# Kernel tuning notes

Measured on AMD Instinct MI355X. Metric: run time of the kernel, lower is better.

## Reference

```python
import jax, jax.numpy as jnp
import numpy as np

N_EMBED = 1024
CUTOFFS = [20000, 60000, 180000]
N_VOCAB = 267735
BOUNDS = [0] + CUTOFFS + [N_VOCAB]            # cluster boundaries
N_EMBEDS = [1024, 256, 64, 16]                # n_embed / 4**i
N_TOK = 1024
N_CLUSTERS = len(CUTOFFS)                      # 3 tail clusters


def setup_inputs() -> dict:
    key = jax.random.key(0)
    ks = jax.random.split(key, 12)

    def w(k, shape):
        fan_in = shape[0]
        return (jax.random.normal(k, shape, jnp.float32) / np.sqrt(fan_in)).astype(jnp.float32)

    inp = {}
    inp["hidden"] = jax.random.normal(ks[0], (N_TOK, N_EMBED), jnp.float32)
    inp["target"] = jax.random.randint(ks[1], (N_TOK,), 0, N_VOCAB)
    # head: layers[0] = Linear(n_embed, cutoffs[0]); clusters = Linear(n_embed, n_clusters)
    inp["W_head"] = w(ks[2], (N_EMBED, BOUNDS[1]))
    inp["b_head"] = jnp.zeros((BOUNDS[1],), jnp.float32)
    inp["W_cluster"] = w(ks[3], (N_EMBED, N_CLUSTERS))
    inp["b_cluster"] = jnp.zeros((N_CLUSTERS,), jnp.float32)
    # tails: projections[i-1] = Linear(n_embed, n_embeds[i], bias=False); layers[i] = Linear(n_embeds[i], end-start)
    for i in range(1, N_CLUSTERS + 1):
        size = BOUNDS[i + 1] - BOUNDS[i]
        inp[f"W_proj{i}"] = w(ks[3 + 2 * i], (N_EMBED, N_EMBEDS[i]))
        inp[f"W_tail{i}"] = w(ks[4 + 2 * i], (N_EMBEDS[i], size))
        inp[f"b_tail{i}"] = jnp.zeros((size,), jnp.float32)
    return inp


def _adaptive_nll(hidden, target, W_head, b_head, W_cluster, b_cluster, tails):
    # head logits = [vocab cluster 0 | cluster logits], then log_softmax (matches torch.cat + log_softmax)
    head_logit = jnp.concatenate(
        [hidden @ W_head + b_head, hidden @ W_cluster + b_cluster], axis=1)  # [N, cut0 + n_clusters]
    head_lp = jax.nn.log_softmax(head_logit, axis=1)

    # cluster 0: logprob = head_lp[n, target]
    t0 = jnp.clip(target, 0, BOUNDS[1] - 1)
    lp0 = jnp.take_along_axis(head_lp, t0[:, None], axis=1)[:, 0]
    nll = jnp.where(target < BOUNDS[1], -lp0, jnp.zeros((), head_lp.dtype))

    # tail clusters i=1..3: logprob = head_lp[:, -i] + tail_log_softmax[n, target-start]
    for i, (Wp, Wt, bt) in enumerate(tails, start=1):
        start, end = BOUNDS[i], BOUNDS[i + 1]
        tail_lp = jax.nn.log_softmax((hidden @ Wp) @ Wt + bt, axis=1)  # [N, end-start]
        rel = jnp.clip(target - start, 0, end - start - 1)
        lp_i = head_lp[:, -i] + jnp.take_along_axis(tail_lp, rel[:, None], axis=1)[:, 0]
        in_bucket = (target >= start) & (target < end)
        nll = jnp.where(in_bucket, -lp_i, nll)
    return nll  # [N], per-token negative log-likelihood (keep_order=True semantics)


def reference(hidden, target, W_head, b_head, W_cluster, b_cluster,
              W_proj1, W_tail1, b_tail1,
              W_proj2, W_tail2, b_tail2,
              W_proj3, W_tail3, b_tail3):
    tails = [(W_proj1, W_tail1, b_tail1),
             (W_proj2, W_tail2, b_tail2),
             (W_proj3, W_tail3, b_tail3)]
    return _adaptive_nll(hidden, target, W_head, b_head, W_cluster, b_cluster, tails)
```

## Files before the change

kernel.cpp:

```cpp
#include <hip/hip_runtime.h>
#include <cstdint>
#include <cstddef>


typedef unsigned short u16;
typedef __attribute__((ext_vector_type(8))) __bf16 bf16x8;
typedef __attribute__((ext_vector_type(8))) u16 u16x8;
typedef __attribute__((ext_vector_type(4))) float f32x4;

#define AS1 __attribute__((address_space(1)))
#define AS3 __attribute__((address_space(3)))

__device__ __forceinline__ u16 f2bf(float f){
  union { float f; unsigned u; } v; v.f = f;
  unsigned r = v.u + 0x7fffu + ((v.u >> 16) & 1u);
  return (u16)(r >> 16);
}
__device__ __forceinline__ void glds16(const void* g, void* l){
  __builtin_amdgcn_global_load_lds((AS1 unsigned*)(uintptr_t)g,
                                   (AS3 unsigned*)(unsigned)(uintptr_t)l, 16, 0, 0);
}

__global__ void k_init(int* __restrict__ cnt, int* __restrict__ trel){
  int i = blockIdx.x * 256 + threadIdx.x;
  trel[i] = -1;
  if (i < 4) cnt[i] = 0;
}

struct TJob { const float* W; u16* BT; int K, N, Kpad, nrows, nx, base, blk; };
struct TJobs { TJob j[8]; int nj; };

template<int TPB>
__device__ __forceinline__ void transpose_tile(const TJobs& jobs, int id,
                                               float (*t)[65], int tid){
  int ji = 0;
  #pragma unroll
  for (int i = 1; i < 8; ++i)
    if (i < jobs.nj && id >= jobs.j[i].base) ji = i;
  TJob jb = jobs.j[ji];
  int local = id - jb.base;
  int bx = local % jb.nx;
  int by = local / jb.nx;

  const int n0 = bx * 64;
  const int k0 = by * 64;
  const bool al = (jb.N & 3) == 0;
  for (int i = tid; i < 64*16; i += TPB){
    int r = i >> 4, c4 = (i & 15) * 4;
    int k = k0 + r, n = n0 + c4;
    f32x4 v; v.x=0.f; v.y=0.f; v.z=0.f; v.w=0.f;
    if (k < jb.K){
      if (al && n + 3 < jb.N) v = *(const f32x4*)(jb.W + (size_t)k * jb.N + n);
      else { for (int q = 0; q < 4; ++q) if (n + q < jb.N) v[q] = jb.W[(size_t)k * jb.N + n + q]; }
    }
    t[r][c4] = v.x; t[r][c4+1] = v.y; t[r][c4+2] = v.z; t[r][c4+3] = v.w;
  }
  __syncthreads();
  for (int i = tid; i < 64*8; i += TPB){
    int rn = i >> 3, c8 = (i & 7) * 8;
    int n = n0 + rn;
    if (k0 + c8 < jb.Kpad && n < jb.nrows){
      u16x8 o;
      #pragma unroll
      for (int q = 0; q < 8; ++q) o[q] = f2bf(t[c8 + q][rn]);
      size_t off;
      if (jb.blk)
        off = (((size_t)(n >> 7) * (jb.Kpad >> 6) + (k0 >> 6)) * 128 + (n & 127)) * 64 + c8;
      else
        off = (size_t)n * jb.Kpad + k0 + c8;
      *(u16x8*)(jb.BT + off) = o;
    }
  }
}

__global__ void k_stage1(TJobs jobs, int nbT, int ncvt,
                         const float* __restrict__ h, u16* __restrict__ a0,
                         const int* __restrict__ tgt, int* __restrict__ cnt,
                         int* __restrict__ idx1, int* __restrict__ idx2,
                         int* __restrict__ idx3, int* __restrict__ pos,
                         int* __restrict__ tr0, int* __restrict__ tr1,
                         int* __restrict__ tr2, int* __restrict__ tr3){
  __shared__ float t[64][65];
  const int bid = blockIdx.x, tid = threadIdx.x;
  if (bid < nbT){
    transpose_tile<256>(jobs, bid, t, tid);
  } else if (bid < nbT + ncvt){
    int i = ((bid - nbT) * 256 + tid) * 8;
    f32x4 v0 = *(const f32x4*)(h + i);
    f32x4 v1 = *(const f32x4*)(h + i + 4);
    u16x8 o;
    o[0]=f2bf(v0.x); o[1]=f2bf(v0.y); o[2]=f2bf(v0.z); o[3]=f2bf(v0.w);
    o[4]=f2bf(v1.x); o[5]=f2bf(v1.y); o[6]=f2bf(v1.z); o[7]=f2bf(v1.w);
    *(u16x8*)(a0 + i) = o;
  } else {
    int n = (bid - nbT - ncvt) * 256 + tid;
    int tv = tgt[n];
    int p = 0;
    tr0[n] = (tv < 20000) ? tv : -1;
    if (tv >= 20000){
      int b = (tv < 60000) ? 0 : (tv < 180000 ? 1 : 2);
      p = atomicAdd(&cnt[b], 1);
      if (b == 0){ idx1[p] = n; tr1[p] = tv - 20000; }
      else if (b == 1){ idx2[p] = n; tr2[p] = tv - 60000; }
      else { idx3[p] = n; tr3[p] = tv - 180000; }
    }
    pos[n] = p;
  }
}

__device__ __forceinline__
void proj_body(const u16* __restrict__ A, const u16* __restrict__ BT,
               const float* __restrict__ bc,
               u16* __restrict__ A1, u16* __restrict__ A2,
               u16* __restrict__ A3, float* __restrict__ cl,
               int pm, int pn, u16* As, u16* Bs)
{
  constexpr int BK = 64, K = 1024;
  const int tid  = threadIdx.x;
  const int lane = tid & 63, wid = tid >> 6;
  const int wm = wid & 3, wn = wid >> 2;
  const int l15 = lane & 15, l4 = lane >> 4;
  const int m0 = pm * 256;
  const int n0 = pn * 128;

  f32x4 acc[4][4];
  #pragma unroll
  for (int m = 0; m < 4; ++m)
    #pragma unroll
    for (int n = 0; n < 4; ++n){ acc[m][n].x=0.f; acc[m][n].y=0.f; acc[m][n].z=0.f; acc[m][n].w=0.f; }

  for (int kt = 0; kt < K / BK; ++kt){
    #pragma unroll
    for (int i = 0; i < 4; ++i){
      int c = wid * 4 + i;
      int row = c * 8 + lane / 8, kb = lane % 8;
      glds16((const char*)(A + (size_t)(m0 + row) * K + kt * BK) + kb * 16,
             (char*)As + c * 1024);
    }
    #pragma unroll
    for (int i = 0; i < 2; ++i){
      int c = wid * 2 + i;
      int row = c * 8 + lane / 8, kb = lane % 8;
      glds16((const char*)(BT + (size_t)(n0 + row) * K + kt * BK) + kb * 16,
             (char*)Bs + c * 1024);
    }
    __syncthreads();
    #pragma unroll
    for (int ks = 0; ks < 2; ++ks){
      bf16x8 af[4], bfr[4];
      #pragma unroll
      for (int m = 0; m < 4; ++m)
        af[m] = *(const bf16x8*)((const char*)As + (wm*64 + m*16 + l15) * (BK*2) + ks*64 + l4*16);
      #pragma unroll
      for (int n = 0; n < 4; ++n)
        bfr[n] = *(const bf16x8*)((const char*)Bs + (wn*64 + n*16 + l15) * (BK*2) + ks*64 + l4*16);
      #pragma unroll
      for (int m = 0; m < 4; ++m)
        #pragma unroll
        for (int n = 0; n < 4; ++n)
          acc[m][n] = __builtin_amdgcn_mfma_f32_16x16x32_bf16(af[m], bfr[n], acc[m][n], 0, 0, 0);
    }
    __syncthreads();
  }
  #pragma unroll
  for (int m = 0; m < 4; ++m)
    #pragma unroll
    for (int n = 0; n < 4; ++n)
      #pragma unroll
      for (int q = 0; q < 4; ++q){
        int c = n0 + wn*64 + n*16 + l15;
        int r = m0 + wm*64 + m*16 + l4*4 + q;
        float v = acc[m][n][q];
        if (c < 256)      A1[(size_t)r*256 + c] = f2bf(v);
        else if (c < 320) A2[(size_t)r*64 + (c-256)] = f2bf(v);
        else if (c < 336){ u16* p = A3 + (size_t)r*32 + (c-320);
                           p[0] = f2bf(v); p[16] = 0; }
        else if (c < 339) cl[(size_t)r*3 + (c-336)] = v + bc[c-336];
      }
}

__device__ __forceinline__
void gemm256_body(const u16* __restrict__ A, const u16* __restrict__ BT,
                  const float* __restrict__ bias, int K, int N,
                  float* __restrict__ P, int ntiles, int cb, int rb,
                  const int* __restrict__ tgt_rel, float* __restrict__ tl,
                  u16* As, u16* Bs, float* reds, int* trel_s)
{
  constexpr int BK = 64;
  const int tid  = threadIdx.x;
  const int lane = tid & 63, wid = tid >> 6;
  const int wm = wid & 3, wn = wid >> 2;
  const int l15 = lane & 15, l4 = lane >> 4;
  const int m0 = rb * 256;
  const int n0 = cb * 128;
  const int srow = lane >> 3, skb = lane & 7;

  if (tid < 256) trel_s[tid] = tgt_rel[m0 + tid];

  f32x4 acc[4][4];
  #pragma unroll
  for (int m = 0; m < 4; ++m)
    #pragma unroll
    for (int n = 0; n < 4; ++n){ acc[m][n].x=0.f; acc[m][n].y=0.f; acc[m][n].z=0.f; acc[m][n].w=0.f; }

  const int ksteps = K / BK;
  for (int kt = 0; kt < ksteps; ++kt){
    #pragma unroll
    for (int i = 0; i < 4; ++i){
      int c = wid * 4 + i;
      int row = c * 8 + srow;
      int kbs = skb ^ (row & 7);
      glds16((const char*)(A + (size_t)(m0 + row) * K + kt * BK) + kbs * 16,
             (char*)As + c * 1024);
    }
    #pragma unroll
    for (int i = 0; i < 2; ++i){
      int c = wid * 2 + i;
      int row = c * 8 + srow;
      int kbs = skb ^ (row & 7);
      glds16((const char*)(BT + ((size_t)(cb * ksteps + kt) * 128 + row) * 64) + kbs * 16,
             (char*)Bs + c * 1024);
    }
    __syncthreads();
    #pragma unroll
    for (int ks = 0; ks < 2; ++ks){
      bf16x8 af[4], bfr[4];
      #pragma unroll
      for (int m = 0; m < 4; ++m){
        int r = wm*64 + m*16 + l15;
        af[m] = *(const bf16x8*)((const char*)As + r*128 + (((ks*4 + l4) ^ (r & 7)) * 16));
      }
      #pragma unroll
      for (int n = 0; n < 4; ++n){
        int r = wn*64 + n*16 + l15;
        bfr[n] = *(const bf16x8*)((const char*)Bs + r*128 + (((ks*4 + l4) ^ (r & 7)) * 16));
      }
      #pragma unroll
      for (int m = 0; m < 4; ++m)
        #pragma unroll
        for (int n = 0; n < 4; ++n)
          acc[m][n] = __builtin_amdgcn_mfma_f32_16x16x32_bf16(af[m], bfr[n], acc[m][n], 0, 0, 0);
    }
    __syncthreads();
  }

  float bv[4]; bool val[4];
  #pragma unroll
  for (int n = 0; n < 4; ++n){
    int col = n0 + wn*64 + n*16 + l15;
    val[n] = col < N;
    bv[n] = val[n] ? bias[col] : 0.f;
  }
  #pragma unroll
  for (int m = 0; m < 4; ++m)
    #pragma unroll
    for (int q = 0; q < 4; ++q){
      int lrow = wm*64 + m*16 + l4*4 + q;
      int tr = trel_s[lrow];
      float Sl = 0.f;
      #pragma unroll
      for (int n = 0; n < 4; ++n){
        if (val[n]){
          float lg = acc[m][n][q] + bv[n];
          Sl += __expf(lg);
          int col = n0 + wn*64 + n*16 + l15;
          if (tr == col) tl[m0 + lrow] = lg;
        }
      }
      #pragma unroll
      for (int d = 1; d < 16; d <<= 1) Sl += __shfl_xor(Sl, d);
      if (l15 == 0) reds[wn*256 + lrow] = Sl;
    }
  __syncthreads();
  if (wn == 0 && l15 == 0){
    #pragma unroll
    for (int m = 0; m < 4; ++m)
      #pragma unroll
      for (int q = 0; q < 4; ++q){
        int lrow = wm*64 + m*16 + l4*4 + q;
        P[(size_t)(m0 + lrow) * ntiles + cb] = reds[lrow] + reds[256 + lrow];
      }
  }
}

__global__ __launch_bounds__(512)
void k_gemm_lse256(const u16* __restrict__ A, const u16* __restrict__ BT,
                   const float* __restrict__ bias, int K, int N,
                   float* __restrict__ P, int ntiles,
                   const int* __restrict__ tgt_rel, float* __restrict__ tl)
{
  __shared__ u16 As[256 * 64];
  __shared__ u16 Bs[128 * 64];
  __shared__ float reds[2 * 256];
  __shared__ int trel_s[256];
  gemm256_body(A, BT, bias, K, N, P, ntiles, blockIdx.x, blockIdx.y,
               tgt_rel, tl, As, Bs, reds, trel_s);
}

__global__ __launch_bounds__(512)
void k_proj_gemm(const u16* __restrict__ A, const u16* __restrict__ BT,
                 const float* __restrict__ bc,
                 u16* __restrict__ A1, u16* __restrict__ A2,
                 u16* __restrict__ A3, float* __restrict__ cl)
{
  __shared__ u16 As[256 * 64];
  __shared__ u16 Bs[128 * 64];
  proj_body(A, BT, bc, A1, A2, A3, cl, blockIdx.y, blockIdx.x, As, Bs);
}

__global__ __launch_bounds__(512)
void k_mega(const u16* __restrict__ A, const u16* __restrict__ BT,
            const float* __restrict__ bias, int ntiles,
            float* __restrict__ P, const int* __restrict__ tgt_rel,
            float* __restrict__ tl, int gb, TJobs tails)
{
  __shared__ __align__(16) char smem[52224];
  const int bid = blockIdx.x;
  if (bid < gb){
    const int q = gb >> 3, r = gb & 7;
    const int xcd = bid & 7, ii = bid >> 3;
    const int swz = (xcd < r ? xcd * (q + 1) : r * (q + 1) + (xcd - r) * q) + ii;
    const int cb = swz >> 2, rb = swz & 3;
    u16* As = (u16*)smem;
    u16* Bs = (u16*)(smem + 32768);
    float* reds = (float*)(smem + 49152);
    int* trel_s = (int*)(smem + 51200);
    gemm256_body(A, BT, bias, 1024, 20000, P, ntiles,
                 cb, rb, tgt_rel, tl, As, Bs, reds, trel_s);
  } else {
    float (*t)[65] = (float(*)[65])smem;
    transpose_tile<512>(tails, bid - gb, t, threadIdx.x);
  }
}

__global__ __launch_bounds__(256)
void k_tail1(const u16* __restrict__ A, const u16* __restrict__ BT,
             const float* __restrict__ bias, int K, int N,
             float* __restrict__ P, int ntiles,
             const int* __restrict__ cnt, int bucket,
             const int* __restrict__ trel, const int* __restrict__ ridx,
             float* __restrict__ tl)
{
  constexpr int BK = 64;
  const int cntv = cnt[bucket];
  const int rb = blockIdx.y, cb = blockIdx.x;
  const int m0 = rb * 128;
  if (m0 >= cntv) return;

  __shared__ u16 As[128 * BK];
  __shared__ u16 Bs[128 * BK];
  __shared__ float reds[2 * 128];
  __shared__ int trel_s[128];

  const int tid  = threadIdx.x;
  const int lane = tid & 63, wid = tid >> 6;
  const int wm = wid & 1, wn = wid >> 1;
  const int l15 = lane & 15, l4 = lane >> 4;
  const int n0 = cb * 128;
  const int srow = lane >> 3, skb = lane & 7;

  if (tid < 128) trel_s[tid] = trel[m0 + tid];

  f32x4 acc[4][4];
  #pragma unroll
  for (int m = 0; m < 4; ++m)
    #pragma unroll
    for (int n = 0; n < 4; ++n){ acc[m][n].x=0.f; acc[m][n].y=0.f; acc[m][n].z=0.f; acc[m][n].w=0.f; }

  const int ksteps = K / BK;
  for (int kt = 0; kt < ksteps; ++kt){
    #pragma unroll
    for (int i = 0; i < 4; ++i){
      int c = wid * 4 + i;
      int row = c * 8 + srow;
      int grow = (m0 + row < cntv) ? ridx[m0 + row] : ridx[0];
      int kbs = skb ^ (row & 7);
      glds16((const char*)(A + (size_t)grow * K + kt * BK) + kbs * 16,
             (char*)As + c * 1024);
    }
    #pragma unroll
    for (int i = 0; i < 4; ++i){
      int c = wid * 4 + i;
      int row = c * 8 + srow;
      int kbs = skb ^ (row & 7);
      glds16((const char*)(BT + ((size_t)(cb * ksteps + kt) * 128 + row) * 64) + kbs * 16,
             (char*)Bs + c * 1024);
    }
    __syncthreads();
    #pragma unroll
    for (int ks = 0; ks < 2; ++ks){
      bf16x8 af[4], bfr[4];
      #pragma unroll
      for (int m = 0; m < 4; ++m){
        int r = wm*64 + m*16 + l15;
        af[m] = *(const bf16x8*)((const char*)As + r*128 + (((ks*4 + l4) ^ (r & 7)) * 16));
      }
      #pragma unroll
      for (int n = 0; n < 4; ++n){
        int r = wn*64 + n*16 + l15;
        bfr[n] = *(const bf16x8*)((const char*)Bs + r*128 + (((ks*4 + l4) ^ (r & 7)) * 16));
      }
      #pragma unroll
      for (int m = 0; m < 4; ++m)
        #pragma unroll
        for (int n = 0; n < 4; ++n)
          acc[m][n] = __builtin_amdgcn_mfma_f32_16x16x32_bf16(af[m], bfr[n], acc[m][n], 0, 0, 0);
    }
    __syncthreads();
  }

  float bv[4]; bool val[4];
  #pragma unroll
  for (int n = 0; n < 4; ++n){
    int col = n0 + wn*64 + n*16 + l15;
    val[n] = col < N;
    bv[n] = val[n] ? bias[col] : 0.f;
  }
  #pragma unroll
  for (int m = 0; m < 4; ++m)
    #pragma unroll
    for (int q = 0; q < 4; ++q){
      int lrow = wm*64 + m*16 + l4*4 + q;
      int tr = trel_s[lrow];
      float Sl = 0.f;
      #pragma unroll
      for (int n = 0; n < 4; ++n){
        if (val[n]){
          float lg = acc[m][n][q] + bv[n];
          Sl += __expf(lg);
          int col = n0 + wn*64 + n*16 + l15;
          if (tr == col) tl[ridx[m0 + lrow]] = lg;
        }
      }
      #pragma unroll
      for (int d = 1; d < 16; d <<= 1) Sl += __shfl_xor(Sl, d);
      if (l15 == 0) reds[wn*128 + lrow] = Sl;
    }
  __syncthreads();
  if (wn == 0 && l15 == 0){
    #pragma unroll
    for (int m = 0; m < 4; ++m)
      #pragma unroll
      for (int q = 0; q < 4; ++q){
        int lrow = wm*64 + m*16 + l4*4 + q;
        P[(size_t)(m0 + lrow) * ntiles + cb] = reds[lrow] + reds[128 + lrow];
      }
  }
}

template<int NC, int BK>
__global__ __launch_bounds__(256)
void k_tail_s(const u16* __restrict__ A, const u16* __restrict__ BT,
              const float* __restrict__ bias, int N,
              float* __restrict__ P, int ntiles,
              const int* __restrict__ cnt, int bucket,
              const int* __restrict__ trel, const int* __restrict__ ridx,
              float* __restrict__ tl)
{
  constexpr int CH  = BK / 8;
  constexpr int LPR = CH;
  constexpr int RPC = 64 / LPR;
  constexpr int CPW = (128 * BK * 2 / 1024) / 4;
  const int cntv = cnt[bucket];
  const int yb = blockIdx.y, cg = blockIdx.x;
  const int m0 = yb * 128;
  if (m0 >= cntv) return;

  __shared__ u16 As[128 * BK];
  __shared__ u16 BsM[2][128 * BK];
  __shared__ float reds[2 * 128];
  __shared__ int trel_s[128];

  const int tid  = threadIdx.x;
  const int lane = tid & 63, wid = tid >> 6;
  const int wm = wid & 1, wn = wid >> 1;
  const int l15 = lane & 15, l4 = lane >> 4;
  const int srow = lane / LPR, skb = lane % LPR;

  if (tid < 128) trel_s[tid] = trel[m0 + tid];

  #pragma unroll
  for (int i = 0; i < CPW; ++i){
    int c = wid * CPW + i;
    int row = c * RPC + srow;
    int grow = (m0 + row < cntv) ? ridx[m0 + row] : ridx[0];
    int kbs = skb ^ (row & (CH - 1));
    glds16((const char*)(A + (size_t)grow * BK) + kbs * 16,
           (char*)As + c * 1024);
  }
  {
    int ci0 = cg * NC;
    if (ci0 < ntiles){
      #pragma unroll
      for (int i = 0; i < CPW; ++i){
        int c = wid * CPW + i;
        int row = c * RPC + srow;
        int kbs = skb ^ (row & (CH - 1));
        glds16((const char*)(BT + (size_t)(ci0*128 + row) * BK) + kbs * 16,
               (char*)BsM[0] + c * 1024);
      }
    }
  }
  __syncthreads();

  int buf = 0;
  for (int ct = 0; ct < NC; ++ct){
    int ci = cg * NC + ct;
    if (ci >= ntiles) break;
    if (ct + 1 < NC && ci + 1 < ntiles){
      #pragma unroll
      for (int i = 0; i < CPW; ++i){
        int c = wid * CPW + i;
        int row = c * RPC + srow;
        int kbs = skb ^ (row & (CH - 1));
        glds16((const char*)(BT + (size_t)((ci+1)*128 + row) * BK) + kbs * 16,
               (char*)BsM[buf ^ 1] + c * 1024);
      }
    }
    f32x4 acc[4][4];
    #pragma unroll
    for (int m = 0; m < 4; ++m)
      #pragma unroll
      for (int n = 0; n < 4; ++n){ acc[m][n].x=0.f; acc[m][n].y=0.f; acc[m][n].z=0.f; acc[m][n].w=0.f; }
    #pragma unroll
    for (int ks = 0; ks < BK / 32; ++ks){
      bf16x8 af[4], bfr[4];
      #pragma unroll
      for (int m = 0; m < 4; ++m){
        int r = wm*64 + m*16 + l15;
        af[m] = *(const bf16x8*)((const char*)As + r*(BK*2) + (((ks*4 + l4) ^ (r & (CH-1))) * 16));
      }
      #pragma unroll
      for (int n = 0; n < 4; ++n){
        int r = wn*64 + n*16 + l15;
        bfr[n] = *(const bf16x8*)((const char*)BsM[buf] + r*(BK*2) + (((ks*4 + l4) ^ (r & (CH-1))) * 16));
      }
      #pragma unroll
      for (int m = 0; m < 4; ++m)
        #pragma unroll
        for (int n = 0; n < 4; ++n)
          acc[m][n] = __builtin_amdgcn_mfma_f32_16x16x32_bf16(af[m], bfr[n], acc[m][n], 0, 0, 0);
    }
    const int n0 = ci * 128;
    float bv[4]; bool val[4];
    #pragma unroll
    for (int n = 0; n < 4; ++n){
      int col = n0 + wn*64 + n*16 + l15;
      val[n] = col < N;
      bv[n] = val[n] ? bias[col] : 0.f;
    }
    #pragma unroll
    for (int m = 0; m < 4; ++m)
      #pragma unroll
      for (int q = 0; q < 4; ++q){
        int lrow = wm*64 + m*16 + l4*4 + q;
        int tr = trel_s[lrow];
        float Sl = 0.f;
        #pragma unroll
        for (int n = 0; n < 4; ++n){
          if (val[n]){
            float lg = acc[m][n][q] + bv[n];
            Sl += __expf(lg);
            int col = n0 + wn*64 + n*16 + l15;
            if (tr == col) tl[ridx[m0 + lrow]] = lg;
          }
        }
        #pragma unroll
        for (int d = 1; d < 16; d <<= 1) Sl += __shfl_xor(Sl, d);
        if (l15 == 0) reds[wn*128 + lrow] = Sl;
      }
    __syncthreads();
    if (wn == 0 && l15 == 0){
      #pragma unroll
      for (int m = 0; m < 4; ++m)
        #pragma unroll
        for (int q = 0; q < 4; ++q){
          int lrow = wm*64 + m*16 + l4*4 + q;
          P[(size_t)(m0 + lrow) * ntiles + ci] = reds[lrow] + reds[128 + lrow];
        }
    }
    __syncthreads();
    buf ^= 1;
  }
}

__global__ void k_finalize(const int* __restrict__ tgt, const float* __restrict__ P,
                           const float* __restrict__ cl, const float* __restrict__ tl,
                           const int* __restrict__ pos, float* __restrict__ out)
{
  const int NT0 = 157, NT1 = 313, NT2 = 938, NT3 = 686;
  int n = blockIdx.x * 4 + (threadIdx.x >> 6);
  int lane = threadIdx.x & 63;
  int t = tgt[n];

  float s = 0.f;
  const float* p0 = P + (size_t)n * NT0;
  for (int i = lane; i < NT0; i += 64) s += p0[i];
  if (lane < 3) s += __expf(cl[n*3 + lane]);
  #pragma unroll
  for (int d = 1; d < 64; d <<= 1) s += __shfl_xor(s, d);
  float lse_head = logf(s);

  float nll;
  if (t < 20000){
    nll = lse_head - tl[n];
  } else {
    int seg, nt; size_t base;
    if      (t <  60000){ seg = 1; nt = NT1; base = (size_t)1024 * NT0; }
    else if (t < 180000){ seg = 2; nt = NT2; base = (size_t)1024 * (NT0 + NT1); }
    else                { seg = 3; nt = NT3; base = (size_t)1024 * (NT0 + NT1 + NT2); }
    float s2 = 0.f;
    const float* ps = P + base + (size_t)pos[n] * nt;
    for (int i = lane; i < nt; i += 64) s2 += ps[i];
    #pragma unroll
    for (int d = 1; d < 64; d <<= 1) s2 += __shfl_xor(s2, d);
    float lse_t = logf(s2);
    nll = lse_head - cl[n*3 + (3 - seg)] + lse_t - tl[n];
  }
  if (lane == 0) out[n] = nll;
}

extern "C" void kernel_launch(void* const* d_in, const int* in_sizes, int n_in,
                              void* d_out, int out_size, void* d_ws, size_t ws_size,
                              hipStream_t stream)
{
  const float* hidden = (const float*)d_in[0];
  const int*   target = (const int*)d_in[1];
  const float* W_head = (const float*)d_in[2];
  const float* b_head = (const float*)d_in[3];
  const float* W_clu  = (const float*)d_in[4];
  const float* b_clu  = (const float*)d_in[5];
  const float* W_p1   = (const float*)d_in[6];
  const float* W_t1   = (const float*)d_in[7];
  const float* b_t1   = (const float*)d_in[8];
  const float* W_p2   = (const float*)d_in[9];
  const float* W_t2   = (const float*)d_in[10];
  const float* b_t2   = (const float*)d_in[11];
  const float* W_p3   = (const float*)d_in[12];
  const float* W_t3   = (const float*)d_in[13];
  const float* b_t3   = (const float*)d_in[14];
  float* out = (float*)d_out;

  char* ws = (char*)d_ws;
  u16*   A0  = (u16*)(ws + 0);
  u16*   A1  = (u16*)(ws + 2097152);
  u16*   A2  = (u16*)(ws + 2621440);
  u16*   A3  = (u16*)(ws + 2752512);
  float* cl  = (float*)(ws + 2883584);
  float* tl  = (float*)(ws + 2895872);
  float* P   = (float*)(ws + 2899968);
  u16*   BTpOv = (u16*)(ws + 2899968);
  u16*   BTh = (u16*)(ws + 11476992);
  int*   cnt  = (int*)(ws + 52633600);
  int*   idx1 = (int*)(ws + 52633856);
  int*   idx2 = (int*)(ws + 52637952);
  int*   idx3 = (int*)(ws + 52642048);
  int*   pos  = (int*)(ws + 52646144);
  int*   trel = (int*)(ws + 52650240);
  int*   tr0 = trel, *tr1 = trel + 1024, *tr2 = trel + 2048, *tr3 = trel + 3072;
  u16*   BT1  = (u16*)(ws + 52666624);
  u16*   BT2  = (u16*)(ws + 73179392);
  u16*   BT3  = (u16*)(ws + 88547584);
  u16*   BTpD = (u16*)(ws + 94167296);
  const size_t needA = 94986496;
  const bool bigws = ws_size >= needA;
  u16* BTp = bigws ? BTpD : BTpOv;

  float* P0  = P;
  float* Pp1 = P + (size_t)1024 * 157;
  float* Pp2 = P + (size_t)1024 * (157 + 313);
  float* Pp3 = P + (size_t)1024 * (157 + 313 + 938);

  auto addj = [](TJobs& tj, int& nb, const float* W, u16* B, int K, int N,
                 int Kpad, int nrows, int blk){
    int nx = (nrows + 63) / 64;
    int ny = (Kpad + 63) / 64;
    tj.j[tj.nj++] = TJob{W, B, K, N, Kpad, nrows, nx, nb, blk};
    nb += nx * ny;
  };

  k_init<<<16, 256, 0, stream>>>(cnt, trel);

  TJobs tj{}; int nb = 0;
  addj(tj, nb, W_p1, BTp, 1024, 256, 1024, 256, 0);
  addj(tj, nb, W_p2, BTp + (size_t)256*1024, 1024, 64, 1024, 64, 0);
  addj(tj, nb, W_p3, BTp + (size_t)320*1024, 1024, 16, 1024, 16, 0);
  addj(tj, nb, W_clu, BTp + (size_t)336*1024, 1024, 3, 1024, 64, 0);
  addj(tj, nb, W_head, BTh, 1024, 20000, 1024, 20096, 1);
  k_stage1<<<nb + 512 + 4, 256, 0, stream>>>(tj, nb, 512, hidden, A0, target,
      cnt, idx1, idx2, idx3, pos, tr0, tr1, tr2, tr3);

  k_proj_gemm<<<dim3(3, 4), 512, 0, stream>>>(A0, BTp, b_clu, A1, A2, A3, cl);

  if (bigws){
    TJobs tt{}; int nbT = 0;
    addj(tt, nbT, W_t1, BT1, 256, 40000, 256, 40064, 1);
    addj(tt, nbT, W_t2, BT2, 64, 120000, 64, 120064, 0);
    addj(tt, nbT, W_t3, BT3, 16, 87735, 32, 87808, 0);
    const int gb = 157 * 4;
    k_mega<<<gb + nbT, 512, 0, stream>>>(A0, BTh, b_head, 157, P0, tr0, tl, gb, tt);

    k_tail1<<<dim3(313, 8), 256, 0, stream>>>(A1, BT1, b_t1, 256, 40000,
        Pp1, 313, cnt, 0, tr1, idx1, tl);
    k_tail_s<4, 64><<<dim3(235, 8), 256, 0, stream>>>(A2, BT2, b_t2, 120000,
        Pp2, 938, cnt, 1, tr2, idx2, tl);
    k_tail_s<4, 32><<<dim3(172, 8), 256, 0, stream>>>(A3, BT3, b_t3, 87735,
        Pp3, 686, cnt, 2, tr3, idx3, tl);
  } else {
    k_gemm_lse256<<<dim3(157, 4), 512, 0, stream>>>(A0, BTh, b_head, 1024, 20000,
        P0, 157, tr0, tl);

    TJobs s1{}; int n1 = 0;
    addj(s1, n1, W_t1, BTh, 256, 40000, 256, 40064, 1);
    k_stage1<<<n1, 256, 0, stream>>>(s1, n1, 0, hidden, A0, target,
        cnt, idx1, idx2, idx3, pos, tr0, tr1, tr2, tr3);
    k_tail1<<<dim3(313, 8), 256, 0, stream>>>(A1, BTh, b_t1, 256, 40000,
        Pp1, 313, cnt, 0, tr1, idx1, tl);

    TJobs s2{}; int n2 = 0;
    addj(s2, n2, W_t2, BTh, 64, 120000, 64, 120064, 0);
    k_stage1<<<n2, 256, 0, stream>>>(s2, n2, 0, hidden, A0, target,
        cnt, idx1, idx2, idx3, pos, tr0, tr1, tr2, tr3);
    k_tail_s<4, 64><<<dim3(235, 8), 256, 0, stream>>>(A2, BTh, b_t2, 120000,
        Pp2, 938, cnt, 1, tr2, idx2, tl);

    TJobs s3{}; int n3 = 0;
    addj(s3, n3, W_t3, BTh, 16, 87735, 32, 87808, 0);
    k_stage1<<<n3, 256, 0, stream>>>(s3, n3, 0, hidden, A0, target,
        cnt, idx1, idx2, idx3, pos, tr0, tr1, tr2, tr3);
    k_tail_s<4, 32><<<dim3(172, 8), 256, 0, stream>>>(A3, BTh, b_t3, 87735,
        Pp3, 686, cnt, 2, tr3, idx3, tl);
  }

  k_finalize<<<256, 256, 0, stream>>>(target, P, cl, tl, pos, out);
}
```

Before: 256.5 us.

## Overlap head-weight transpose tail with projection GEMM; split preprocessing kernel

Preprocessing is split into a separate k_pre kernel for the bf16 conversion and target bucketing, and k_init is replaced by a memset of the counters. In the default path the W_head transpose now covers only the first 17024 columns before the projection GEMM. The remaining columns are transposed by extra blocks launched in the same kernel as the 12-block projection GEMM, so idle CUs do useful work during that small GEMM. To support the partial transpose, TJob gains a leading-dimension field. The trel=-1 init is dropped, and tail kernels now guard target writes with a row-count check, which adds a kernel launch and a little index logic.

```diff
diff --git a/kernel.cpp b/kernel.cpp
--- a/kernel.cpp
+++ b/kernel.cpp
@@ -21,13 +21,7 @@
                                    (AS3 unsigned*)(unsigned)(uintptr_t)l, 16, 0, 0);
 }
 
-__global__ void k_init(int* __restrict__ cnt, int* __restrict__ trel){
-  int i = blockIdx.x * 256 + threadIdx.x;
-  trel[i] = -1;
-  if (i < 4) cnt[i] = 0;
-}
-
-struct TJob { const float* W; u16* BT; int K, N, Kpad, nrows, nx, base, blk; };
+struct TJob { const float* W; u16* BT; int K, N, ldw, Kpad, nrows, nx, base, blk; };
 struct TJobs { TJob j[8]; int nj; };
 
 template<int TPB>
@@ -50,8 +44,8 @@
     int k = k0 + r, n = n0 + c4;
     f32x4 v; v.x=0.f; v.y=0.f; v.z=0.f; v.w=0.f;
     if (k < jb.K){
-      if (al && n + 3 < jb.N) v = *(const f32x4*)(jb.W + (size_t)k * jb.N + n);
-      else { for (int q = 0; q < 4; ++q) if (n + q < jb.N) v[q] = jb.W[(size_t)k * jb.N + n + q]; }
+      if (al && n + 3 < jb.N) v = *(const f32x4*)(jb.W + (size_t)k * jb.ldw + n);
+      else { for (int q = 0; q < 4; ++q) if (n + q < jb.N) v[q] = jb.W[(size_t)k * jb.ldw + n + q]; }
     }
     t[r][c4] = v.x; t[r][c4+1] = v.y; t[r][c4+2] = v.z; t[r][c4+3] = v.w;
   }
@@ -73,19 +67,15 @@
   }
 }
 
-__global__ void k_stage1(TJobs jobs, int nbT, int ncvt,
-                         const float* __restrict__ h, u16* __restrict__ a0,
-                         const int* __restrict__ tgt, int* __restrict__ cnt,
-                         int* __restrict__ idx1, int* __restrict__ idx2,
-                         int* __restrict__ idx3, int* __restrict__ pos,
-                         int* __restrict__ tr0, int* __restrict__ tr1,
-                         int* __restrict__ tr2, int* __restrict__ tr3){
-  __shared__ float t[64][65];
+__global__ void k_pre(const float* __restrict__ h, u16* __restrict__ a0,
+                      const int* __restrict__ tgt, int* __restrict__ cnt,
+                      int* __restrict__ idx1, int* __restrict__ idx2,
+                      int* __restrict__ idx3, int* __restrict__ pos,
+                      int* __restrict__ tr0, int* __restrict__ tr1,
+                      int* __restrict__ tr2, int* __restrict__ tr3){
   const int bid = blockIdx.x, tid = threadIdx.x;
-  if (bid < nbT){
-    transpose_tile<256>(jobs, bid, t, tid);
-  } else if (bid < nbT + ncvt){
-    int i = ((bid - nbT) * 256 + tid) * 8;
+  if (bid < 512){
+    int i = (bid * 256 + tid) * 8;
     f32x4 v0 = *(const f32x4*)(h + i);
     f32x4 v1 = *(const f32x4*)(h + i + 4);
     u16x8 o;
@@ -93,7 +83,7 @@
     o[4]=f2bf(v1.x); o[5]=f2bf(v1.y); o[6]=f2bf(v1.z); o[7]=f2bf(v1.w);
     *(u16x8*)(a0 + i) = o;
   } else {
-    int n = (bid - nbT - ncvt) * 256 + tid;
+    int n = (bid - 512) * 256 + tid;
     int tv = tgt[n];
     int p = 0;
     tr0[n] = (tv < 20000) ? tv : -1;
@@ -108,6 +98,11 @@
   }
 }
 
+__global__ void k_stage1(TJobs jobs){
+  __shared__ float t[64][65];
+  transpose_tile<256>(jobs, blockIdx.x, t, threadIdx.x);
+}
+
 __device__ __forceinline__
 void proj_body(const u16* __restrict__ A, const u16* __restrict__ BT,
                const float* __restrict__ bc,
@@ -179,6 +174,23 @@
       }
 }
 
+__global__ __launch_bounds__(512)
+void k_proj_plus(const u16* __restrict__ A, const u16* __restrict__ BT,
+                 const float* __restrict__ bc,
+                 u16* __restrict__ A1, u16* __restrict__ A2,
+                 u16* __restrict__ A3, float* __restrict__ cl, TJobs fill)
+{
+  __shared__ __align__(16) char smem[49152];
+  const int bid = blockIdx.x;
+  if (bid < 12){
+    proj_body(A, BT, bc, A1, A2, A3, cl, bid / 3, bid % 3,
+              (u16*)smem, (u16*)(smem + 32768));
+  } else {
+    float (*t)[65] = (float(*)[65])smem;
+    transpose_tile<512>(fill, bid - 12, t, threadIdx.x);
+  }
+}
+
 __device__ __forceinline__
 void gemm256_body(const u16* __restrict__ A, const u16* __restrict__ BT,
                   const float* __restrict__ bias, int K, int N,
@@ -295,17 +307,6 @@
   __shared__ int trel_s[256];
   gemm256_body(A, BT, bias, K, N, P, ntiles, blockIdx.x, blockIdx.y,
                tgt_rel, tl, As, Bs, reds, trel_s);
-}
-
-__global__ __launch_bounds__(512)
-void k_proj_gemm(const u16* __restrict__ A, const u16* __restrict__ BT,
-                 const float* __restrict__ bc,
-                 u16* __restrict__ A1, u16* __restrict__ A2,
-                 u16* __restrict__ A3, float* __restrict__ cl)
-{
-  __shared__ u16 As[256 * 64];
-  __shared__ u16 Bs[128 * 64];
-  proj_body(A, BT, bc, A1, A2, A3, cl, blockIdx.y, blockIdx.x, As, Bs);
 }
 
 __global__ __launch_bounds__(512)
@@ -422,6 +423,7 @@
     for (int q = 0; q < 4; ++q){
       int lrow = wm*64 + m*16 + l4*4 + q;
       int tr = trel_s[lrow];
+      bool live = (m0 + lrow) < cntv;
       float Sl = 0.f;
       #pragma unroll
       for (int n = 0; n < 4; ++n){
@@ -429,7 +431,7 @@
           float lg = acc[m][n][q] + bv[n];
           Sl += __expf(lg);
           int col = n0 + wn*64 + n*16 + l15;
-          if (tr == col) tl[ridx[m0 + lrow]] = lg;
+          if (live && tr == col) tl[ridx[m0 + lrow]] = lg;
         }
       }
       #pragma unroll
@@ -555,6 +557,7 @@
       for (int q = 0; q < 4; ++q){
         int lrow = wm*64 + m*16 + l4*4 + q;
         int tr = trel_s[lrow];
+        bool live = (m0 + lrow) < cntv;
         float Sl = 0.f;
         #pragma unroll
         for (int n = 0; n < 4; ++n){
@@ -562,7 +565,7 @@
             float lg = acc[m][n][q] + bv[n];
             Sl += __expf(lg);
             int col = n0 + wn*64 + n*16 + l15;
-            if (tr == col) tl[ridx[m0 + lrow]] = lg;
+            if (live && tr == col) tl[ridx[m0 + lrow]] = lg;
           }
         }
         #pragma unroll
@@ -672,31 +675,35 @@
   float* Pp3 = P + (size_t)1024 * (157 + 313 + 938);
 
   auto addj = [](TJobs& tj, int& nb, const float* W, u16* B, int K, int N,
-                 int Kpad, int nrows, int blk){
+                 int ldw, int Kpad, int nrows, int blk){
     int nx = (nrows + 63) / 64;
     int ny = (Kpad + 63) / 64;
-    tj.j[tj.nj++] = TJob{W, B, K, N, Kpad, nrows, nx, nb, blk};
+    tj.j[tj.nj++] = TJob{W, B, K, N, ldw, Kpad, nrows, nx, nb, blk};
     nb += nx * ny;
   };
 
-  k_init<<<16, 256, 0, stream>>>(cnt, trel);
-
-  TJobs tj{}; int nb = 0;
-  addj(tj, nb, W_p1, BTp, 1024, 256, 1024, 256, 0);
-  addj(tj, nb, W_p2, BTp + (size_t)256*1024, 1024, 64, 1024, 64, 0);
-  addj(tj, nb, W_p3, BTp + (size_t)320*1024, 1024, 16, 1024, 16, 0);
-  addj(tj, nb, W_clu, BTp + (size_t)336*1024, 1024, 3, 1024, 64, 0);
-  addj(tj, nb, W_head, BTh, 1024, 20000, 1024, 20096, 1);
-  k_stage1<<<nb + 512 + 4, 256, 0, stream>>>(tj, nb, 512, hidden, A0, target,
-      cnt, idx1, idx2, idx3, pos, tr0, tr1, tr2, tr3);
-
-  k_proj_gemm<<<dim3(3, 4), 512, 0, stream>>>(A0, BTp, b_clu, A1, A2, A3, cl);
+  hipMemsetAsync(cnt, 0, 16, stream);
+  k_pre<<<516, 256, 0, stream>>>(hidden, A0, target, cnt,
+                                 idx1, idx2, idx3, pos, tr0, tr1, tr2, tr3);
 
   if (bigws){
+    TJobs tj{}; int nb = 0;
+    addj(tj, nb, W_p1, BTp, 1024, 256, 256, 1024, 256, 0);
+    addj(tj, nb, W_p2, BTp + (size_t)256*1024, 1024, 64, 64, 1024, 64, 0);
+    addj(tj, nb, W_p3, BTp + (size_t)320*1024, 1024, 16, 16, 1024, 16, 0);
+    addj(tj, nb, W_clu, BTp + (size_t)336*1024, 1024, 3, 3, 1024, 64, 0);
+    addj(tj, nb, W_head, BTh, 1024, 20000, 20000, 1024, 17024, 1);
+    k_stage1<<<nb, 256, 0, stream>>>(tj);
+
+    TJobs fj{}; int nf = 0;
+    addj(fj, nf, W_head + 17024, BTh + (size_t)133*131072, 1024,
+         20000 - 17024 , 20000, 1024, 20096 - 17024 , 1);
+    k_proj_plus<<<12 + nf, 512, 0, stream>>>(A0, BTp, b_clu, A1, A2, A3, cl, fj);
+
     TJobs tt{}; int nbT = 0;
-    addj(tt, nbT, W_t1, BT1, 256, 40000, 256, 40064, 1);
-    addj(tt, nbT, W_t2, BT2, 64, 120000, 64, 120064, 0);
-    addj(tt, nbT, W_t3, BT3, 16, 87735, 32, 87808, 0);
+    addj(tt, nbT, W_t1, BT1, 256, 40000, 40000, 256, 40064, 1);
+    addj(tt, nbT, W_t2, BT2, 64, 120000, 120000, 64, 120064, 0);
+    addj(tt, nbT, W_t3, BT3, 16, 87735, 87735, 32, 87808, 0);
     const int gb = 157 * 4;
     k_mega<<<gb + nbT, 512, 0, stream>>>(A0, BTh, b_head, 157, P0, tr0, tl, gb, tt);
 
@@ -707,27 +714,35 @@
     k_tail_s<4, 32><<<dim3(172, 8), 256, 0, stream>>>(A3, BT3, b_t3, 87735,
         Pp3, 686, cnt, 2, tr3, idx3, tl);
   } else {
+    TJobs tj{}; int nb = 0;
+    addj(tj, nb, W_p1, BTp, 1024, 256, 256, 1024, 256, 0);
+    addj(tj, nb, W_p2, BTp + (size_t)256*1024, 1024, 64, 64, 1024, 64, 0);
+    addj(tj, nb, W_p3, BTp + (size_t)320*1024, 1024, 16, 16, 1024, 16, 0);
+    addj(tj, nb, W_clu, BTp + (size_t)336*1024, 1024, 3, 3, 1024, 64, 0);
+    addj(tj, nb, W_head, BTh, 1024, 20000, 20000, 1024, 20096, 1);
+    k_stage1<<<nb, 256, 0, stream>>>(tj);
+
+    TJobs fj0{};
+    k_proj_plus<<<12, 512, 0, stream>>>(A0, BTp, b_clu, A1, A2, A3, cl, fj0);
+
     k_gemm_lse256<<<dim3(157, 4), 512, 0, stream>>>(A0, BTh, b_head, 1024, 20000,
         P0, 157, tr0, tl);
 
     TJobs s1{}; int n1 = 0;
-    addj(s1, n1, W_t1, BTh, 256, 40000, 256, 40064, 1);
-    k_stage1<<<n1, 256, 0, stream>>>(s1, n1, 0, hidden, A0, target,
-        cnt, idx1, idx2, idx3, pos, tr0, tr1, tr2, tr3);
+    addj(s1, n1, W_t1, BTh, 256, 40000, 40000, 256, 40064, 1);
+    k_stage1<<<n1, 256, 0, stream>>>(s1);
     k_tail1<<<dim3(313, 8), 256, 0, stream>>>(A1, BTh, b_t1, 256, 40000,
         Pp1, 313, cnt, 0, tr1, idx1, tl);
 
     TJobs s2{}; int n2 = 0;
-    addj(s2, n2, W_t2, BTh, 64, 120000, 64, 120064, 0);
-    k_stage1<<<n2, 256, 0, stream>>>(s2, n2, 0, hidden, A0, target,
-        cnt, idx1, idx2, idx3, pos, tr0, tr1, tr2, tr3);
+    addj(s2, n2, W_t2, BTh, 64, 120000, 120000, 64, 120064, 0);
+    k_stage1<<<n2, 256, 0, stream>>>(s2);
     k_tail_s<4, 64><<<dim3(235, 8), 256, 0, stream>>>(A2, BTh, b_t2, 120000,
         Pp2, 938, cnt, 1, tr2, idx2, tl);
 
     TJobs s3{}; int n3 = 0;
-    addj(s3, n3, W_t3, BTh, 16, 87735, 32, 87808, 0);
-    k_stage1<<<n3, 256, 0, stream>>>(s3, n3, 0, hidden, A0, target,
-        cnt, idx1, idx2, idx3, pos, tr0, tr1, tr2, tr3);
+    addj(s3, n3, W_t3, BTh, 16, 87735, 87735, 32, 87808, 0);
+    k_stage1<<<n3, 256, 0, stream>>>(s3);
     k_tail_s<4, 32><<<dim3(172, 8), 256, 0, stream>>>(A3, BTh, b_t3, 87735,
         Pp3, 686, cnt, 2, tr3, idx3, tl);
   }
```

New measurement: 257.2 us. Within noise of the previous version (+0.3%).
